# Kernel tuning notes

Measured on AMD Instinct MI355X. Metric: run time of the kernel, lower is better.

Reference implementation:

```python
import jax, jax.numpy as jnp
import numpy as np

N = 50000      # num nodes
E = 1_600_000  # num edges (avg degree 32)
IN = 128       # in_dim
HID = 64       # hidden_dim
H = 4          # heads (layer 1)
NEG_SLOPE = 0.2


def setup_inputs() -> dict:
    key = jax.random.key(0)
    ks = jax.random.split(key, 20)
    g = lambda k, s: jax.random.normal(k, s, dtype=jnp.float32) * 0.05
    return {
        "x": jax.random.normal(ks[0], (N, IN), dtype=jnp.float32),
        "edge_index": jax.random.randint(ks[1], (2, E), 0, N, dtype=jnp.int32),
        # GATv2 layer 1: in=128 -> heads=4, out=64, concat -> 256
        "W1l": g(ks[2], (IN, H * HID)), "b1l": g(ks[3], (H * HID,)),
        "W1r": g(ks[4], (IN, H * HID)), "b1r": g(ks[5], (H * HID,)),
        "att1": g(ks[6], (H, HID)),     "bias1": g(ks[7], (H * HID,)),
        # GATv2 layer 2: in=256 -> heads=1, out=64
        "W2l": g(ks[8], (H * HID, HID)), "b2l": g(ks[9], (HID,)),
        "W2r": g(ks[10], (H * HID, HID)), "b2r": g(ks[11], (HID,)),
        "att2": g(ks[12], (1, HID)),     "bias2": g(ks[13], (HID,)),
        # readout: 64 -> 1
        "Wro": g(ks[14], (HID, 1)), "bro": g(ks[15], (1,)),
    }


def gatv2_layer(x, src, dst, Wl, bl, Wr, br, att, bias, heads, out_ch, concat):
    n = x.shape[0]
    xl = (x @ Wl + bl).reshape(n, heads, out_ch)  # source transform [N,H,C]
    xr = (x @ Wr + br).reshape(n, heads, out_ch)  # target transform [N,H,C]
    # per-edge GATv2 score: a^T LeakyReLU(xl_j + xr_i)
    e = jax.nn.leaky_relu(xl[src] + xr[dst], NEG_SLOPE)      # [E,H,C]
    score = jnp.einsum('ehc,hc->eh', e, att)                 # [E,H]
    # segment softmax over edges sharing the same target node
    m = jax.ops.segment_max(score, dst, num_segments=n)      # [N,H]
    a = jnp.exp(score - m[dst])                              # [E,H]
    denom = jax.ops.segment_sum(a, dst, num_segments=n)      # [N,H]
    alpha = a / denom[dst]
    # weighted scatter-add of source messages
    out = jax.ops.segment_sum(xl[src] * alpha[:, :, None], dst, num_segments=n)  # [N,H,C]
    out = out.reshape(n, heads * out_ch) if concat else out.mean(axis=1)
    return out + bias


def reference(x, edge_index, W1l, b1l, W1r, b1r, att1, bias1,
              W2l, b2l, W2r, b2r, att2, bias2, Wro, bro):
    src, dst = edge_index[0], edge_index[1]
    h = gatv2_layer(x, src, dst, W1l, b1l, W1r, b1r, att1, bias1, H, HID, True)
    h = jax.nn.elu(h)
    h = gatv2_layer(h, src, dst, W2l, b2l, W2r, b2r, att2, bias2, 1, HID, True)
    h = jax.nn.elu(h)
    return h @ Wro + bro  # [N, 1]
```

## Files before the change

### kernel.cpp

```cpp
#include <hip/hip_runtime.h>
#include <hip/hip_bf16.h>
#include <cstdint>
#include <cstddef>

#define NEG_SLOPE 0.2f
#define LOG2E 1.4426950408889634f
#define NBKT 196
#define BCAP 10000
#define P1CHUNK 4096

typedef __attribute__((ext_vector_type(8))) short bf16x8;
typedef __attribute__((ext_vector_type(4))) float f32x4;

__device__ __forceinline__ unsigned short f2bf(float f) {
  unsigned u = __float_as_uint(f);
  u = u + 0x7FFFu + ((u >> 16) & 1u);
  return (unsigned short)(u >> 16);
}
__device__ __forceinline__ unsigned pack2bf(float a, float b) {
  return (unsigned)f2bf(a) | ((unsigned)f2bf(b) << 16);
}
__device__ __forceinline__ float4 cvt_bf4(uint2 q) {
  float4 v;
  v.x = __uint_as_float(q.x << 16);
  v.y = __uint_as_float(q.x & 0xffff0000u);
  v.z = __uint_as_float(q.y << 16);
  v.w = __uint_as_float(q.y & 0xffff0000u);
  return v;
}

__global__ void fill_u32(unsigned* __restrict__ p, unsigned v, long long n) {
  long long i = (long long)blockIdx.x * blockDim.x + threadIdx.x;
  long long s = (long long)gridDim.x * blockDim.x;
  for (; i < n; i += s) p[i] = v;
}

__global__ __launch_bounds__(256) void csr_p1(const int* __restrict__ src,
                                              const int* __restrict__ dst,
                                              int* __restrict__ bcnt,
                                              unsigned* __restrict__ stage, int E) {
  __shared__ int cnt[NBKT], gbase[NBKT];
  const int t = threadIdx.x;
  const int e0 = blockIdx.x * P1CHUNK;
  const int e1 = min(e0 + P1CHUNK, E);
  for (int i = t; i < NBKT; i += 256) cnt[i] = 0;
  __syncthreads();
  for (int e = e0 + t; e < e1; e += 256) atomicAdd(&cnt[dst[e] >> 8], 1);
  __syncthreads();
  for (int i = t; i < NBKT; i += 256) {
    gbase[i] = cnt[i] ? atomicAdd(&bcnt[i], cnt[i]) : 0;
    cnt[i] = 0;
  }
  __syncthreads();
  for (int e = e0 + t; e < e1; e += 256) {
    const int d = dst[e];
    const int b = d >> 8;
    const int r = gbase[b] + atomicAdd(&cnt[b], 1);
    if (r < BCAP)
      stage[(size_t)b * BCAP + r] = (unsigned)src[e] | ((unsigned)(d & 255) << 24);
  }
}

__global__ __launch_bounds__(1024) void csr_p2(const unsigned* __restrict__ stage,
                                               const int* __restrict__ bcnt,
                                               int* __restrict__ csr_src,
                                               int* __restrict__ base, int N, int E) {
  __shared__ int h[256], c[256];
  __shared__ int allb[NBKT];
  __shared__ int ob_s;
  const int t = threadIdx.x;
  const int b = blockIdx.x;
  if (t < 256) h[t] = 0;
  for (int i = t; i < NBKT; i += 1024) allb[i] = min(bcnt[i], BCAP);
  __syncthreads();
  if (t == 0) {
    int s = 0;
    for (int i = 0; i < b; ++i) s += allb[i];
    ob_s = s;
  }
  __syncthreads();
  const int out_base = ob_s;
  const int cnt = allb[b];
  const unsigned* sp = stage + (size_t)b * BCAP;
  for (int i = t; i < cnt; i += 1024) atomicAdd(&h[sp[i] >> 24], 1);
  __syncthreads();
  const int own = (t < 256) ? h[t] : 0;
  for (int off = 1; off < 256; off <<= 1) {
    const int add = (t < 256 && t >= off) ? h[t - off] : 0;
    __syncthreads();
    if (t < 256) h[t] += add;
    __syncthreads();
  }
  if (t < 256) {
    const int excl = h[t] - own;
    c[t] = excl;
    const int node = b * 256 + t;
    if (node < N) base[node] = out_base + excl;
  }
  if (b == gridDim.x - 1 && t == 0) base[N] = E;
  __syncthreads();
  for (int i = t; i < cnt; i += 1024) {
    const unsigned v = sp[i];
    const int pos = out_base + atomicAdd(&c[v >> 24], 1);
    csr_src[pos] = (int)(v & 0xFFFFFFu);
  }
}

__device__ __forceinline__ void wt_cvt(const float* __restrict__ Wl,
                                       const float* __restrict__ Wr,
                                       unsigned short* __restrict__ Wt, int K, int C, int idx) {
  const int k = idx / (2 * C);
  const int c = idx - k * 2 * C;
  const float v = (c < C) ? Wl[(size_t)k * C + c] : Wr[(size_t)k * C + (c - C)];
  Wt[(size_t)c * K + k] = f2bf(v);
}

__global__ void prep(const float* __restrict__ x,
                     const float* __restrict__ W1l, const float* __restrict__ W1r,
                     const float* __restrict__ W2l, const float* __restrict__ W2r,
                     unsigned short* __restrict__ xbf, unsigned short* __restrict__ Wt1,
                     unsigned short* __restrict__ Wt2, long long n8) {
  const int b = blockIdx.x;
  const int t = threadIdx.x;
  if (b < 2048) {
    long long i = (long long)b * 256 + t;
    const long long s = 2048LL * 256;
    for (; i < n8; i += s) {
      const float4 a = ((const float4*)x)[i * 2];
      const float4 c = ((const float4*)x)[i * 2 + 1];
      ((uint2*)xbf)[i * 2] = make_uint2(pack2bf(a.x, a.y), pack2bf(a.z, a.w));
      ((uint2*)xbf)[i * 2 + 1] = make_uint2(pack2bf(c.x, c.y), pack2bf(c.z, c.w));
    }
  } else if (b < 2304) {
    wt_cvt(W1l, W1r, Wt1, 128, 256, (b - 2048) * 256 + t);
  } else {
    wt_cvt(W2l, W2r, Wt2, 256, 64, (b - 2304) * 256 + t);
  }
}

template <int K, int NT, int SPLIT>
__global__ __launch_bounds__(256) void gemm_mfma(
    const unsigned short* __restrict__ A, const unsigned short* __restrict__ Wt,
    const float* __restrict__ bl, const float* __restrict__ br,
    unsigned short* __restrict__ Yl, unsigned short* __restrict__ Yr) {
  constexpr int KS = K / 32;
  constexpr int CW = NT / 4;
  constexpr int NTILES = CW / 16;
  const int wv = threadIdx.x >> 6, lane = threadIdx.x & 63;
  const int n0 = blockIdx.x * 16;
  const int ar = lane & 15;
  const int kg = lane >> 4;

  bf16x8 afrag[KS];
#pragma unroll
  for (int ks = 0; ks < KS; ++ks)
    afrag[ks] = *(const bf16x8*)(A + (size_t)(n0 + ar) * K + ks * 32 + kg * 8);

  const int col0w = wv * CW;
#pragma unroll
  for (int nt = 0; nt < NTILES; ++nt) {
    const int c0 = col0w + nt * 16;
    const int ccol = c0 + (lane & 15);
    f32x4 acc = {0.f, 0.f, 0.f, 0.f};
#pragma unroll
    for (int ks = 0; ks < KS; ++ks) {
      const bf16x8 bfrag = *(const bf16x8*)(Wt + (size_t)ccol * K + ks * 32 + kg * 8);
      acc = __builtin_amdgcn_mfma_f32_16x16x32_bf16(afrag[ks], bfrag, acc, 0, 0, 0);
    }
    if (c0 < SPLIT) {
      const float bv = bl[ccol];
#pragma unroll
      for (int j = 0; j < 4; ++j) {
        const int node = n0 + (lane >> 4) * 4 + j;
        Yl[(size_t)node * SPLIT + ccol] = f2bf(acc[j] + bv);
      }
    } else {
      const float bv = br[ccol - SPLIT];
#pragma unroll
      for (int j = 0; j < 4; ++j) {
        const int node = n0 + (lane >> 4) * 4 + j;
        Yr[(size_t)node * (NT - SPLIT) + (ccol - SPLIT)] = f2bf(acc[j] + bv);
      }
    }
  }
}

__device__ __forceinline__ float edge_p(const float4 c, const float4 xrv, const float4 attv) {
  const float v0 = c.x + xrv.x, v1 = c.y + xrv.y, v2 = c.z + xrv.z, v3 = c.w + xrv.w;
  float p = fmaxf(v0, v0 * NEG_SLOPE) * attv.x;
  p = fmaf(fmaxf(v1, v1 * NEG_SLOPE), attv.y, p);
  p = fmaf(fmaxf(v2, v2 * NEG_SLOPE), attv.z, p);
  p = fmaf(fmaxf(v3, v3 * NEG_SLOPE), attv.w, p);
  p += __shfl_xor(p, 1);
  p += __shfl_xor(p, 2);
  p += __shfl_xor(p, 4);
  p += __shfl_xor(p, 8);
  return __builtin_amdgcn_exp2f(p);
}

__device__ __forceinline__ void edge_acc(uint2 c, const float4& xrv, const float4& attv,
                                         float& dsum, float4& acc) {
  const float4 x = cvt_bf4(c);
  const float p = edge_p(x, xrv, attv);
  dsum += p;
  acc.x = fmaf(p, x.x, acc.x);
  acc.y = fmaf(p, x.y, acc.y);
  acc.z = fmaf(p, x.z, acc.z);
  acc.w = fmaf(p, x.w, acc.w);
}

__global__ __launch_bounds__(256) void node_l1_fused(
    const unsigned short* __restrict__ xlb, const unsigned short* __restrict__ xrb,
    const int* __restrict__ csr_src, const int* __restrict__ base,
    const float* __restrict__ att, const float* __restrict__ bias,
    unsigned short* __restrict__ outb, int N) {
  const int wv = threadIdx.x >> 6, lane = threadIdx.x & 63;
  const int n = blockIdx.x * 4 + wv;
  if (n >= N) return;
  const int beg = __builtin_amdgcn_readfirstlane(base[n]);
  const int deg = __builtin_amdgcn_readfirstlane(base[n + 1]) - beg;
  const float4 xrv = cvt_bf4(((const uint2*)xrb)[(size_t)n * 64 + lane]);
  float4 attv = ((const float4*)att)[lane];
  attv.x *= LOG2E; attv.y *= LOG2E; attv.z *= LOG2E; attv.w *= LOG2E;

  float dsum = 0.f;
  float4 acc = make_float4(0.f, 0.f, 0.f, 0.f);

  if (deg > 0) {
    const int dm1 = deg - 1;
    const uint2* XL = (const uint2*)xlb;
    int s0 = csr_src[beg];
    int s1 = csr_src[beg + (1 < dm1 ? 1 : dm1)];
    int s2 = csr_src[beg + (2 < dm1 ? 2 : dm1)];
    int s3 = csr_src[beg + (3 < dm1 ? 3 : dm1)];
    uint2 r0 = XL[(size_t)s0 * 64 + lane];
    uint2 r1 = XL[(size_t)s1 * 64 + lane];
    uint2 r2 = XL[(size_t)s2 * 64 + lane];
    uint2 r3 = XL[(size_t)s3 * 64 + lane];
    s0 = csr_src[beg + (4 < dm1 ? 4 : dm1)];
    s1 = csr_src[beg + (5 < dm1 ? 5 : dm1)];
    s2 = csr_src[beg + (6 < dm1 ? 6 : dm1)];
    s3 = csr_src[beg + (7 < dm1 ? 7 : dm1)];
    for (int i = 0; i < deg; i += 4) {
      const uint2 c0 = r0, c1 = r1, c2 = r2, c3 = r3;
      r0 = XL[(size_t)s0 * 64 + lane];
      r1 = XL[(size_t)s1 * 64 + lane];
      r2 = XL[(size_t)s2 * 64 + lane];
      r3 = XL[(size_t)s3 * 64 + lane];
      const int j0 = i + 8 < dm1 ? i + 8 : dm1;
      const int j1 = i + 9 < dm1 ? i + 9 : dm1;
      const int j2 = i + 10 < dm1 ? i + 10 : dm1;
      const int j3 = i + 11 < dm1 ? i + 11 : dm1;
      s0 = csr_src[beg + j0];
      s1 = csr_src[beg + j1];
      s2 = csr_src[beg + j2];
      s3 = csr_src[beg + j3];
      edge_acc(c0, xrv, attv, dsum, acc);
      if (i + 1 <= dm1) edge_acc(c1, xrv, attv, dsum, acc);
      if (i + 2 <= dm1) edge_acc(c2, xrv, attv, dsum, acc);
      if (i + 3 <= dm1) edge_acc(c3, xrv, attv, dsum, acc);
    }
  }
  const float inv = (deg > 0) ? 1.0f / dsum : 0.f;
  const float4 b4 = ((const float4*)bias)[lane];
  float4 o;
  o.x = fmaf(acc.x, inv, b4.x); o.x = o.x > 0.f ? o.x : expm1f(o.x);
  o.y = fmaf(acc.y, inv, b4.y); o.y = o.y > 0.f ? o.y : expm1f(o.y);
  o.z = fmaf(acc.z, inv, b4.z); o.z = o.z > 0.f ? o.z : expm1f(o.z);
  o.w = fmaf(acc.w, inv, b4.w); o.w = o.w > 0.f ? o.w : expm1f(o.w);
  ((uint2*)outb)[(size_t)n * 64 + lane] = make_uint2(pack2bf(o.x, o.y), pack2bf(o.z, o.w));
}

__global__ __launch_bounds__(256) void node_l2_fused(
    const unsigned short* __restrict__ xlb, const unsigned short* __restrict__ xrb,
    const int* __restrict__ csr_src, const int* __restrict__ base,
    const float* __restrict__ att, const float* __restrict__ bias,
    const float* __restrict__ Wro, const float* __restrict__ bro,
    float* __restrict__ out, int N) {
  const int gl = threadIdx.x & 15;
  const int n = blockIdx.x * 16 + (threadIdx.x >> 4);
  const int gbase = (threadIdx.x & 63) & 48;
  if (n >= N) return;
  const int beg = base[n];
  const int deg = base[n + 1] - beg;
  const float4 xrv = cvt_bf4(((const uint2*)xrb)[(size_t)n * 16 + gl]);
  float4 attv = ((const float4*)att)[gl];
  attv.x *= LOG2E; attv.y *= LOG2E; attv.z *= LOG2E; attv.w *= LOG2E;
  const uint2* XL = (const uint2*)xlb;

  float dsum = 0.f;
  float4 acc = make_float4(0.f, 0.f, 0.f, 0.f);

  for (int chunk = 0; chunk < deg; chunk += 16) {
    const int cnt = min(16, deg - chunk);
    const int si = (gl < cnt) ? csr_src[beg + chunk + gl] : 0;
    int s = __shfl(si, gbase);
    uint2 nx = XL[(size_t)s * 16 + gl];
    for (int j = 0; j < cnt; ++j) {
      const uint2 cj = nx;
      if (j + 1 < cnt) {
        const int s2 = __shfl(si, gbase + j + 1);
        nx = XL[(size_t)s2 * 16 + gl];
      }
      edge_acc(cj, xrv, attv, dsum, acc);
    }
  }
  const float inv = (deg > 0) ? 1.0f / dsum : 0.f;
  const float4 b4 = ((const float4*)bias)[gl];
  float ox = fmaf(acc.x, inv, b4.x); ox = ox > 0.f ? ox : expm1f(ox);
  float oy = fmaf(acc.y, inv, b4.y); oy = oy > 0.f ? oy : expm1f(oy);
  float oz = fmaf(acc.z, inv, b4.z); oz = oz > 0.f ? oz : expm1f(oz);
  float ow = fmaf(acc.w, inv, b4.w); ow = ow > 0.f ? ow : expm1f(ow);
  const float4 w4 = ((const float4*)Wro)[gl];
  float r = ox * w4.x + oy * w4.y + oz * w4.z + ow * w4.w;
  r += __shfl_xor(r, 1);
  r += __shfl_xor(r, 2);
  r += __shfl_xor(r, 4);
  r += __shfl_xor(r, 8);
  if (gl == 0) out[n] = r + bro[0];
}

extern "C" void kernel_launch(void* const* d_in, const int* in_sizes, int n_in,
                              void* d_out, int out_size, void* d_ws, size_t ws_size,
                              hipStream_t stream) {
  const float* x     = (const float*)d_in[0];
  const int*   ei    = (const int*)d_in[1];
  const float* W1l   = (const float*)d_in[2];
  const float* b1l   = (const float*)d_in[3];
  const float* W1r   = (const float*)d_in[4];
  const float* b1r   = (const float*)d_in[5];
  const float* att1  = (const float*)d_in[6];
  const float* bias1 = (const float*)d_in[7];
  const float* W2l   = (const float*)d_in[8];
  const float* b2l   = (const float*)d_in[9];
  const float* W2r   = (const float*)d_in[10];
  const float* b2r   = (const float*)d_in[11];
  const float* att2  = (const float*)d_in[12];
  const float* bias2 = (const float*)d_in[13];
  const float* Wro   = (const float*)d_in[14];
  const float* bro   = (const float*)d_in[15];

  const int N = in_sizes[0] / 128;
  const int E = in_sizes[1] / 2;
  const int* src = ei;
  const int* dst = ei + E;

  float* ws = (float*)d_ws;
  unsigned short* xbf  = (unsigned short*)ws;
  unsigned short* xl1b = (unsigned short*)(ws + (size_t)64 * N);
  unsigned short* xr1b = (unsigned short*)(ws + (size_t)192 * N);
  unsigned short* h1b  = (unsigned short*)(ws + (size_t)320 * N);
  int* csr_src = (int*)(ws + (size_t)448 * N);
  int* base    = csr_src + E;
  int* bcnt    = base + N + 1;
  unsigned* stage = (unsigned*)(bcnt + NBKT);
  unsigned short* Wt1 = (unsigned short*)(stage + (size_t)NBKT * BCAP);
  unsigned short* Wt2 = Wt1 + 512 * 128;
  unsigned short* xl2b = xbf;
  unsigned short* xr2b = xl1b;

  fill_u32<<<dim3(1), dim3(256), 0, stream>>>((unsigned*)bcnt, 0u, NBKT);
  csr_p1<<<dim3((E + P1CHUNK - 1) / P1CHUNK), dim3(256), 0, stream>>>(src, dst, bcnt, stage, E);
  csr_p2<<<dim3(NBKT), dim3(1024), 0, stream>>>(stage, bcnt, csr_src, base, N, E);

  prep<<<dim3(2432), dim3(256), 0, stream>>>(x, W1l, W1r, W2l, W2r, xbf, Wt1, Wt2,
                                             (long long)N * 128 / 8);

  gemm_mfma<128, 512, 256><<<dim3(N / 16), dim3(256), 0, stream>>>(xbf, Wt1, b1l, b1r,
                                                                   xl1b, xr1b);
  node_l1_fused<<<dim3((N + 3) / 4), dim3(256), 0, stream>>>(xl1b, xr1b, csr_src, base,
                                                             att1, bias1, h1b, N);

  gemm_mfma<256, 128, 64><<<dim3(N / 16), dim3(256), 0, stream>>>(h1b, Wt2, b2l, b2r,
                                                                  xl2b, xr2b);
  node_l2_fused<<<dim3((N + 15) / 16), dim3(256), 0, stream>>>(xl2b, xr2b, csr_src, base,
                                                               att2, bias2, Wro, bro,
                                                               (float*)d_out, N);
}
```

Baseline: 302.5 us.

## Process multiple edges per wavefront in GAT aggregation kernels with wider loads

Layer-1 aggregation now has each wavefront handle two edges at once: each 32-lane half reads 16 bytes per lane from one edge's source row, and the halves are combined with a cross-half shuffle at the end. Layer-2 aggregation moves from 16 nodes per block to one node per wavefront, with four 16-lane quarters each processing a different edge and a reduction across quarters at the end. The aim is more memory-level parallelism and fewer serialized per-edge iterations during the gather. The bounds check on n was removed, which relies on N being a multiple of 4, and layer 2 launches four times as many blocks.

```diff
diff --git a/kernel.cpp b/kernel.cpp
--- a/kernel.cpp
+++ b/kernel.cpp
@@ -20,13 +20,21 @@
 __device__ __forceinline__ unsigned pack2bf(float a, float b) {
   return (unsigned)f2bf(a) | ((unsigned)f2bf(b) << 16);
 }
-__device__ __forceinline__ float4 cvt_bf4(uint2 q) {
-  float4 v;
-  v.x = __uint_as_float(q.x << 16);
-  v.y = __uint_as_float(q.x & 0xffff0000u);
-  v.z = __uint_as_float(q.y << 16);
-  v.w = __uint_as_float(q.y & 0xffff0000u);
-  return v;
+__device__ __forceinline__ void cvt_bf8(uint4 u, float* f) {
+  f[0] = __uint_as_float(u.x << 16);
+  f[1] = __uint_as_float(u.x & 0xffff0000u);
+  f[2] = __uint_as_float(u.y << 16);
+  f[3] = __uint_as_float(u.y & 0xffff0000u);
+  f[4] = __uint_as_float(u.z << 16);
+  f[5] = __uint_as_float(u.z & 0xffff0000u);
+  f[6] = __uint_as_float(u.w << 16);
+  f[7] = __uint_as_float(u.w & 0xffff0000u);
+}
+__device__ __forceinline__ void cvt_bf4p(uint2 u, float* f) {
+  f[0] = __uint_as_float(u.x << 16);
+  f[1] = __uint_as_float(u.x & 0xffff0000u);
+  f[2] = __uint_as_float(u.y << 16);
+  f[3] = __uint_as_float(u.y & 0xffff0000u);
 }
 
 __global__ void fill_u32(unsigned* __restrict__ p, unsigned v, long long n) {
@@ -185,30 +193,6 @@
   }
 }
 
-__device__ __forceinline__ float edge_p(const float4 c, const float4 xrv, const float4 attv) {
-  const float v0 = c.x + xrv.x, v1 = c.y + xrv.y, v2 = c.z + xrv.z, v3 = c.w + xrv.w;
-  float p = fmaxf(v0, v0 * NEG_SLOPE) * attv.x;
-  p = fmaf(fmaxf(v1, v1 * NEG_SLOPE), attv.y, p);
-  p = fmaf(fmaxf(v2, v2 * NEG_SLOPE), attv.z, p);
-  p = fmaf(fmaxf(v3, v3 * NEG_SLOPE), attv.w, p);
-  p += __shfl_xor(p, 1);
-  p += __shfl_xor(p, 2);
-  p += __shfl_xor(p, 4);
-  p += __shfl_xor(p, 8);
-  return __builtin_amdgcn_exp2f(p);
-}
-
-__device__ __forceinline__ void edge_acc(uint2 c, const float4& xrv, const float4& attv,
-                                         float& dsum, float4& acc) {
-  const float4 x = cvt_bf4(c);
-  const float p = edge_p(x, xrv, attv);
-  dsum += p;
-  acc.x = fmaf(p, x.x, acc.x);
-  acc.y = fmaf(p, x.y, acc.y);
-  acc.z = fmaf(p, x.z, acc.z);
-  acc.w = fmaf(p, x.w, acc.w);
-}
-
 __global__ __launch_bounds__(256) void node_l1_fused(
     const unsigned short* __restrict__ xlb, const unsigned short* __restrict__ xrb,
     const int* __restrict__ csr_src, const int* __restrict__ base,
@@ -216,37 +200,125 @@
     unsigned short* __restrict__ outb, int N) {
   const int wv = threadIdx.x >> 6, lane = threadIdx.x & 63;
   const int n = blockIdx.x * 4 + wv;
-  if (n >= N) return;
+  const int h = lane >> 5;
+  const int q = lane & 31;
   const int beg = __builtin_amdgcn_readfirstlane(base[n]);
   const int deg = __builtin_amdgcn_readfirstlane(base[n + 1]) - beg;
-  const float4 xrv = cvt_bf4(((const uint2*)xrb)[(size_t)n * 64 + lane]);
-  float4 attv = ((const float4*)att)[lane];
-  attv.x *= LOG2E; attv.y *= LOG2E; attv.z *= LOG2E; attv.w *= LOG2E;
+  const uint4* XL = (const uint4*)xlb;
+
+  float xr[8];
+  cvt_bf8(((const uint4*)xrb)[(size_t)n * 32 + q], xr);
+  float at[8];
+  {
+    const float4 a0 = ((const float4*)att)[q * 2];
+    const float4 a1 = ((const float4*)att)[q * 2 + 1];
+    at[0] = a0.x * LOG2E; at[1] = a0.y * LOG2E; at[2] = a0.z * LOG2E; at[3] = a0.w * LOG2E;
+    at[4] = a1.x * LOG2E; at[5] = a1.y * LOG2E; at[6] = a1.z * LOG2E; at[7] = a1.w * LOG2E;
+  }
 
   float dsum = 0.f;
-  float4 acc = make_float4(0.f, 0.f, 0.f, 0.f);
+  float acc[8] = {0.f, 0.f, 0.f, 0.f, 0.f, 0.f, 0.f, 0.f};
 
   if (deg > 0) {
     const int dm1 = deg - 1;
-    const uint2* XL = (const uint2*)xlb;
+    int sA = csr_src[beg];
+    int sB = csr_src[beg + (1 < dm1 ? 1 : dm1)];
+    uint4 r = XL[(size_t)(h ? sB : sA) * 32 + q];
+    sA = csr_src[beg + (2 < dm1 ? 2 : dm1)];
+    sB = csr_src[beg + (3 < dm1 ? 3 : dm1)];
+    for (int i = 0; i < deg; i += 2) {
+      const uint4 cur = r;
+      r = XL[(size_t)(h ? sB : sA) * 32 + q];
+      const int j0 = i + 4 < dm1 ? i + 4 : dm1;
+      const int j1 = i + 5 < dm1 ? i + 5 : dm1;
+      sA = csr_src[beg + j0];
+      sB = csr_src[beg + j1];
+      float xl[8];
+      cvt_bf8(cur, xl);
+      float p = 0.f;
+#pragma unroll
+      for (int c = 0; c < 8; ++c) {
+        const float v = xl[c] + xr[c];
+        p = fmaf(fmaxf(v, v * NEG_SLOPE), at[c], p);
+      }
+      p += __shfl_xor(p, 1);
+      p += __shfl_xor(p, 2);
+      p += __shfl_xor(p, 4);
+      p = __builtin_amdgcn_exp2f(p);
+      if (h && (i + 1 > dm1)) p = 0.f;
+      dsum += p;
+#pragma unroll
+      for (int c = 0; c < 8; ++c) acc[c] = fmaf(p, xl[c], acc[c]);
+    }
+    dsum += __shfl_xor(dsum, 32);
+#pragma unroll
+    for (int c = 0; c < 8; ++c) acc[c] += __shfl_xor(acc[c], 32);
+  }
+  const float inv = (deg > 0) ? 1.0f / dsum : 0.f;
+  if (h == 0) {
+    const float4 b0 = ((const float4*)bias)[q * 2];
+    const float4 b1 = ((const float4*)bias)[q * 2 + 1];
+    const float bb[8] = {b0.x, b0.y, b0.z, b0.w, b1.x, b1.y, b1.z, b1.w};
+    float o[8];
+#pragma unroll
+    for (int c = 0; c < 8; ++c) {
+      float v = fmaf(acc[c], inv, bb[c]);
+      o[c] = v > 0.f ? v : expm1f(v);
+    }
+    uint4 pk;
+    pk.x = pack2bf(o[0], o[1]);
+    pk.y = pack2bf(o[2], o[3]);
+    pk.z = pack2bf(o[4], o[5]);
+    pk.w = pack2bf(o[6], o[7]);
+    ((uint4*)outb)[(size_t)n * 32 + q] = pk;
+  }
+}
+
+__global__ __launch_bounds__(256) void node_l2_fused(
+    const unsigned short* __restrict__ xlb, const unsigned short* __restrict__ xrb,
+    const int* __restrict__ csr_src, const int* __restrict__ base,
+    const float* __restrict__ att, const float* __restrict__ bias,
+    const float* __restrict__ Wro, const float* __restrict__ bro,
+    float* __restrict__ out, int N) {
+  const int wv = threadIdx.x >> 6, lane = threadIdx.x & 63;
+  const int n = blockIdx.x * 4 + wv;
+  const int qd = lane >> 4;
+  const int q = lane & 15;
+  const int beg = __builtin_amdgcn_readfirstlane(base[n]);
+  const int deg = __builtin_amdgcn_readfirstlane(base[n + 1]) - beg;
+  const uint2* XL = (const uint2*)xlb;
+
+  float xr[4];
+  cvt_bf4p(((const uint2*)xrb)[(size_t)n * 16 + q], xr);
+  float at[4];
+  {
+    const float4 a = ((const float4*)att)[q];
+    at[0] = a.x * LOG2E; at[1] = a.y * LOG2E; at[2] = a.z * LOG2E; at[3] = a.w * LOG2E;
+  }
+
+  float dsum = 0.f;
+  float acc[4] = {0.f, 0.f, 0.f, 0.f};
+
+  if (deg > 0) {
+    const int dm1 = deg - 1;
     int s0 = csr_src[beg];
     int s1 = csr_src[beg + (1 < dm1 ? 1 : dm1)];
     int s2 = csr_src[beg + (2 < dm1 ? 2 : dm1)];
     int s3 = csr_src[beg + (3 < dm1 ? 3 : dm1)];
-    uint2 r0 = XL[(size_t)s0 * 64 + lane];
-    uint2 r1 = XL[(size_t)s1 * 64 + lane];
-    uint2 r2 = XL[(size_t)s2 * 64 + lane];
-    uint2 r3 = XL[(size_t)s3 * 64 + lane];
+    int sa = (qd & 1) ? s1 : s0;
+    int sb = (qd & 1) ? s3 : s2;
+    int sel = (qd & 2) ? sb : sa;
+    uint2 r = XL[(size_t)sel * 16 + q];
     s0 = csr_src[beg + (4 < dm1 ? 4 : dm1)];
     s1 = csr_src[beg + (5 < dm1 ? 5 : dm1)];
     s2 = csr_src[beg + (6 < dm1 ? 6 : dm1)];
     s3 = csr_src[beg + (7 < dm1 ? 7 : dm1)];
     for (int i = 0; i < deg; i += 4) {
-      const uint2 c0 = r0, c1 = r1, c2 = r2, c3 = r3;
-      r0 = XL[(size_t)s0 * 64 + lane];
-      r1 = XL[(size_t)s1 * 64 + lane];
-      r2 = XL[(size_t)s2 * 64 + lane];
-      r3 = XL[(size_t)s3 * 64 + lane];
+      const uint2 cur = r;
+      sa = (qd & 1) ? s1 : s0;
+      sb = (qd & 1) ? s3 : s2;
+      sel = (qd & 2) ? sb : sa;
+      r = XL[(size_t)sel * 16 + q];
       const int j0 = i + 8 < dm1 ? i + 8 : dm1;
       const int j1 = i + 9 < dm1 ? i + 9 : dm1;
       const int j2 = i + 10 < dm1 ? i + 10 : dm1;
@@ -255,69 +327,49 @@
       s1 = csr_src[beg + j1];
       s2 = csr_src[beg + j2];
       s3 = csr_src[beg + j3];
-      edge_acc(c0, xrv, attv, dsum, acc);
-      if (i + 1 <= dm1) edge_acc(c1, xrv, attv, dsum, acc);
-      if (i + 2 <= dm1) edge_acc(c2, xrv, attv, dsum, acc);
-      if (i + 3 <= dm1) edge_acc(c3, xrv, attv, dsum, acc);
+      float xl[4];
+      cvt_bf4p(cur, xl);
+      float p = 0.f;
+#pragma unroll
+      for (int c = 0; c < 4; ++c) {
+        const float v = xl[c] + xr[c];
+        p = fmaf(fmaxf(v, v * NEG_SLOPE), at[c], p);
+      }
+      p += __shfl_xor(p, 1);
+      p += __shfl_xor(p, 2);
+      p += __shfl_xor(p, 4);
+      p += __shfl_xor(p, 8);
+      p = __builtin_amdgcn_exp2f(p);
+      if (i + qd > dm1) p = 0.f;
+      dsum += p;
+#pragma unroll
+      for (int c = 0; c < 4; ++c) acc[c] = fmaf(p, xl[c], acc[c]);
+    }
+    dsum += __shfl_xor(dsum, 16);
+    dsum += __shfl_xor(dsum, 32);
+#pragma unroll
+    for (int c = 0; c < 4; ++c) {
+      acc[c] += __shfl_xor(acc[c], 16);
+      acc[c] += __shfl_xor(acc[c], 32);
     }
   }
   const float inv = (deg > 0) ? 1.0f / dsum : 0.f;
-  const float4 b4 = ((const float4*)bias)[lane];
-  float4 o;
-  o.x = fmaf(acc.x, inv, b4.x); o.x = o.x > 0.f ? o.x : expm1f(o.x);
-  o.y = fmaf(acc.y, inv, b4.y); o.y = o.y > 0.f ? o.y : expm1f(o.y);
-  o.z = fmaf(acc.z, inv, b4.z); o.z = o.z > 0.f ? o.z : expm1f(o.z);
-  o.w = fmaf(acc.w, inv, b4.w); o.w = o.w > 0.f ? o.w : expm1f(o.w);
-  ((uint2*)outb)[(size_t)n * 64 + lane] = make_uint2(pack2bf(o.x, o.y), pack2bf(o.z, o.w));
-}
-
-__global__ __launch_bounds__(256) void node_l2_fused(
-    const unsigned short* __restrict__ xlb, const unsigned short* __restrict__ xrb,
-    const int* __restrict__ csr_src, const int* __restrict__ base,
-    const float* __restrict__ att, const float* __restrict__ bias,
-    const float* __restrict__ Wro, const float* __restrict__ bro,
-    float* __restrict__ out, int N) {
-  const int gl = threadIdx.x & 15;
-  const int n = blockIdx.x * 16 + (threadIdx.x >> 4);
-  const int gbase = (threadIdx.x & 63) & 48;
-  if (n >= N) return;
-  const int beg = base[n];
-  const int deg = base[n + 1] - beg;
-  const float4 xrv = cvt_bf4(((const uint2*)xrb)[(size_t)n * 16 + gl]);
-  float4 attv = ((const float4*)att)[gl];
-  attv.x *= LOG2E; attv.y *= LOG2E; attv.z *= LOG2E; attv.w *= LOG2E;
-  const uint2* XL = (const uint2*)xlb;
-
-  float dsum = 0.f;
-  float4 acc = make_float4(0.f, 0.f, 0.f, 0.f);
-
-  for (int chunk = 0; chunk < deg; chunk += 16) {
-    const int cnt = min(16, deg - chunk);
-    const int si = (gl < cnt) ? csr_src[beg + chunk + gl] : 0;
-    int s = __shfl(si, gbase);
-    uint2 nx = XL[(size_t)s * 16 + gl];
-    for (int j = 0; j < cnt; ++j) {
-      const uint2 cj = nx;
-      if (j + 1 < cnt) {
-        const int s2 = __shfl(si, gbase + j + 1);
-        nx = XL[(size_t)s2 * 16 + gl];
-      }
-      edge_acc(cj, xrv, attv, dsum, acc);
-    }
-  }
-  const float inv = (deg > 0) ? 1.0f / dsum : 0.f;
-  const float4 b4 = ((const float4*)bias)[gl];
-  float ox = fmaf(acc.x, inv, b4.x); ox = ox > 0.f ? ox : expm1f(ox);
-  float oy = fmaf(acc.y, inv, b4.y); oy = oy > 0.f ? oy : expm1f(oy);
-  float oz = fmaf(acc.z, inv, b4.z); oz = oz > 0.f ? oz : expm1f(oz);
-  float ow = fmaf(acc.w, inv, b4.w); ow = ow > 0.f ? ow : expm1f(ow);
-  const float4 w4 = ((const float4*)Wro)[gl];
-  float r = ox * w4.x + oy * w4.y + oz * w4.z + ow * w4.w;
+  const float4 b4 = ((const float4*)bias)[q];
+  const float bb[4] = {b4.x, b4.y, b4.z, b4.w};
+  const float4 w4 = ((const float4*)Wro)[q];
+  const float ww[4] = {w4.x, w4.y, w4.z, w4.w};
+  float r = 0.f;
+#pragma unroll
+  for (int c = 0; c < 4; ++c) {
+    float v = fmaf(acc[c], inv, bb[c]);
+    v = v > 0.f ? v : expm1f(v);
+    r = fmaf(v, ww[c], r);
+  }
   r += __shfl_xor(r, 1);
   r += __shfl_xor(r, 2);
   r += __shfl_xor(r, 4);
   r += __shfl_xor(r, 8);
-  if (gl == 0) out[n] = r + bro[0];
+  if (lane == 0) out[n] = r + bro[0];
 }
 
 extern "C" void kernel_launch(void* const* d_in, const int* in_sizes, int n_in,
@@ -373,7 +425,7 @@
 
   gemm_mfma<256, 128, 64><<<dim3(N / 16), dim3(256), 0, stream>>>(h1b, Wt2, b2l, b2r,
                                                                   xl2b, xr2b);
-  node_l2_fused<<<dim3((N + 15) / 16), dim3(256), 0, stream>>>(xl2b, xr2b, csr_src, base,
-                                                               att2, bias2, Wro, bro,
-                                                               (float*)d_out, N);
-}
+  node_l2_fused<<<dim3((N + 3) / 4), dim3(256), 0, stream>>>(xl2b, xr2b, csr_src, base,
+                                                             att2, bias2, Wro, bro,
+                                                             (float*)d_out, N);
+}
```

Result: slower. 314.0 us (+3.8%).

## Merge independent CSR build and prep/GEMM stages into shared launches

Applied to the files above, without the earlier changes.

The CSR pass-1 bucketing now shares one launch with the bf16 conversion of x and the weights. The CSR pass-2 scatter shares one launch with the layer-1 GEMM, with block ranges picking the role. The fill kernel becomes a hipMemsetAsync. This cuts the launch count and lets independent work run side by side on the GPU instead of serialising. Pass 2 now uses 256-thread blocks instead of 1024, so each bucket gets fewer threads.

```diff
diff --git a/kernel.cpp b/kernel.cpp
--- a/kernel.cpp
+++ b/kernel.cpp
@@ -8,6 +8,7 @@
 #define NBKT 196
 #define BCAP 10000
 #define P1CHUNK 4096
+#define P1B 391
 
 typedef __attribute__((ext_vector_type(8))) short bf16x8;
 typedef __attribute__((ext_vector_type(4))) float f32x4;
@@ -29,83 +30,6 @@
   return v;
 }
 
-__global__ void fill_u32(unsigned* __restrict__ p, unsigned v, long long n) {
-  long long i = (long long)blockIdx.x * blockDim.x + threadIdx.x;
-  long long s = (long long)gridDim.x * blockDim.x;
-  for (; i < n; i += s) p[i] = v;
-}
-
-__global__ __launch_bounds__(256) void csr_p1(const int* __restrict__ src,
-                                              const int* __restrict__ dst,
-                                              int* __restrict__ bcnt,
-                                              unsigned* __restrict__ stage, int E) {
-  __shared__ int cnt[NBKT], gbase[NBKT];
-  const int t = threadIdx.x;
-  const int e0 = blockIdx.x * P1CHUNK;
-  const int e1 = min(e0 + P1CHUNK, E);
-  for (int i = t; i < NBKT; i += 256) cnt[i] = 0;
-  __syncthreads();
-  for (int e = e0 + t; e < e1; e += 256) atomicAdd(&cnt[dst[e] >> 8], 1);
-  __syncthreads();
-  for (int i = t; i < NBKT; i += 256) {
-    gbase[i] = cnt[i] ? atomicAdd(&bcnt[i], cnt[i]) : 0;
-    cnt[i] = 0;
-  }
-  __syncthreads();
-  for (int e = e0 + t; e < e1; e += 256) {
-    const int d = dst[e];
-    const int b = d >> 8;
-    const int r = gbase[b] + atomicAdd(&cnt[b], 1);
-    if (r < BCAP)
-      stage[(size_t)b * BCAP + r] = (unsigned)src[e] | ((unsigned)(d & 255) << 24);
-  }
-}
-
-__global__ __launch_bounds__(1024) void csr_p2(const unsigned* __restrict__ stage,
-                                               const int* __restrict__ bcnt,
-                                               int* __restrict__ csr_src,
-                                               int* __restrict__ base, int N, int E) {
-  __shared__ int h[256], c[256];
-  __shared__ int allb[NBKT];
-  __shared__ int ob_s;
-  const int t = threadIdx.x;
-  const int b = blockIdx.x;
-  if (t < 256) h[t] = 0;
-  for (int i = t; i < NBKT; i += 1024) allb[i] = min(bcnt[i], BCAP);
-  __syncthreads();
-  if (t == 0) {
-    int s = 0;
-    for (int i = 0; i < b; ++i) s += allb[i];
-    ob_s = s;
-  }
-  __syncthreads();
-  const int out_base = ob_s;
-  const int cnt = allb[b];
-  const unsigned* sp = stage + (size_t)b * BCAP;
-  for (int i = t; i < cnt; i += 1024) atomicAdd(&h[sp[i] >> 24], 1);
-  __syncthreads();
-  const int own = (t < 256) ? h[t] : 0;
-  for (int off = 1; off < 256; off <<= 1) {
-    const int add = (t < 256 && t >= off) ? h[t - off] : 0;
-    __syncthreads();
-    if (t < 256) h[t] += add;
-    __syncthreads();
-  }
-  if (t < 256) {
-    const int excl = h[t] - own;
-    c[t] = excl;
-    const int node = b * 256 + t;
-    if (node < N) base[node] = out_base + excl;
-  }
-  if (b == gridDim.x - 1 && t == 0) base[N] = E;
-  __syncthreads();
-  for (int i = t; i < cnt; i += 1024) {
-    const unsigned v = sp[i];
-    const int pos = out_base + atomicAdd(&c[v >> 24], 1);
-    csr_src[pos] = (int)(v & 0xFFFFFFu);
-  }
-}
-
 __device__ __forceinline__ void wt_cvt(const float* __restrict__ Wl,
                                        const float* __restrict__ Wr,
                                        unsigned short* __restrict__ Wt, int K, int C, int idx) {
@@ -115,15 +39,39 @@
   Wt[(size_t)c * K + k] = f2bf(v);
 }
 
-__global__ void prep(const float* __restrict__ x,
-                     const float* __restrict__ W1l, const float* __restrict__ W1r,
-                     const float* __restrict__ W2l, const float* __restrict__ W2r,
-                     unsigned short* __restrict__ xbf, unsigned short* __restrict__ Wt1,
-                     unsigned short* __restrict__ Wt2, long long n8) {
+__global__ __launch_bounds__(256) void k1_csrp1_prep(
+    const int* __restrict__ src, const int* __restrict__ dst,
+    int* __restrict__ bcnt, unsigned* __restrict__ stage, int E,
+    const float* __restrict__ x,
+    const float* __restrict__ W1l, const float* __restrict__ W1r,
+    const float* __restrict__ W2l, const float* __restrict__ W2r,
+    unsigned short* __restrict__ xbf, unsigned short* __restrict__ Wt1,
+    unsigned short* __restrict__ Wt2, long long n8) {
+  __shared__ int cnt[NBKT], gbase[NBKT];
   const int b = blockIdx.x;
   const int t = threadIdx.x;
-  if (b < 2048) {
-    long long i = (long long)b * 256 + t;
+  if (b < P1B) {
+    const int e0 = b * P1CHUNK;
+    const int e1 = min(e0 + P1CHUNK, E);
+    for (int i = t; i < NBKT; i += 256) cnt[i] = 0;
+    __syncthreads();
+    for (int e = e0 + t; e < e1; e += 256) atomicAdd(&cnt[dst[e] >> 8], 1);
+    __syncthreads();
+    for (int i = t; i < NBKT; i += 256) {
+      gbase[i] = cnt[i] ? atomicAdd(&bcnt[i], cnt[i]) : 0;
+      cnt[i] = 0;
+    }
+    __syncthreads();
+    for (int e = e0 + t; e < e1; e += 256) {
+      const int d = dst[e];
+      const int bk = d >> 8;
+      const int r = gbase[bk] + atomicAdd(&cnt[bk], 1);
+      if (r < BCAP)
+        stage[(size_t)bk * BCAP + r] = (unsigned)src[e] | ((unsigned)(d & 255) << 24);
+    }
+  } else if (b < P1B + 2048) {
+    const int lb = b - P1B;
+    long long i = (long long)lb * 256 + t;
     const long long s = 2048LL * 256;
     for (; i < n8; i += s) {
       const float4 a = ((const float4*)x)[i * 2];
@@ -131,23 +79,23 @@
       ((uint2*)xbf)[i * 2] = make_uint2(pack2bf(a.x, a.y), pack2bf(a.z, a.w));
       ((uint2*)xbf)[i * 2 + 1] = make_uint2(pack2bf(c.x, c.y), pack2bf(c.z, c.w));
     }
-  } else if (b < 2304) {
-    wt_cvt(W1l, W1r, Wt1, 128, 256, (b - 2048) * 256 + t);
+  } else if (b < P1B + 2048 + 256) {
+    wt_cvt(W1l, W1r, Wt1, 128, 256, (b - (P1B + 2048)) * 256 + t);
   } else {
-    wt_cvt(W2l, W2r, Wt2, 256, 64, (b - 2304) * 256 + t);
+    wt_cvt(W2l, W2r, Wt2, 256, 64, (b - (P1B + 2048 + 256)) * 256 + t);
   }
 }
 
 template <int K, int NT, int SPLIT>
-__global__ __launch_bounds__(256) void gemm_mfma(
+__device__ __forceinline__ void gemm_body(
     const unsigned short* __restrict__ A, const unsigned short* __restrict__ Wt,
     const float* __restrict__ bl, const float* __restrict__ br,
-    unsigned short* __restrict__ Yl, unsigned short* __restrict__ Yr) {
+    unsigned short* __restrict__ Yl, unsigned short* __restrict__ Yr, int bb) {
   constexpr int KS = K / 32;
   constexpr int CW = NT / 4;
   constexpr int NTILES = CW / 16;
   const int wv = threadIdx.x >> 6, lane = threadIdx.x & 63;
-  const int n0 = blockIdx.x * 16;
+  const int n0 = bb * 16;
   const int ar = lane & 15;
   const int kg = lane >> 4;
 
@@ -183,6 +131,65 @@
       }
     }
   }
+}
+
+__global__ __launch_bounds__(256) void k2_csrp2_gemm1(
+    const unsigned* __restrict__ stage, const int* __restrict__ bcnt,
+    int* __restrict__ csr_src, int* __restrict__ base, int N, int E,
+    const unsigned short* __restrict__ A, const unsigned short* __restrict__ Wt,
+    const float* __restrict__ bl, const float* __restrict__ br,
+    unsigned short* __restrict__ Yl, unsigned short* __restrict__ Yr) {
+  __shared__ int h[256], c[256];
+  __shared__ int allb[NBKT];
+  __shared__ int ob_s;
+  const int b = blockIdx.x;
+  const int t = threadIdx.x;
+  if (b >= NBKT) {
+    gemm_body<128, 512, 256>(A, Wt, bl, br, Yl, Yr, b - NBKT);
+    return;
+  }
+  h[t] = 0;
+  for (int i = t; i < NBKT; i += 256) allb[i] = min(bcnt[i], BCAP);
+  __syncthreads();
+  if (t == 0) {
+    int s = 0;
+    for (int i = 0; i < b; ++i) s += allb[i];
+    ob_s = s;
+  }
+  __syncthreads();
+  const int out_base = ob_s;
+  const int cnt = allb[b];
+  const unsigned* sp = stage + (size_t)b * BCAP;
+  for (int i = t; i < cnt; i += 256) atomicAdd(&h[sp[i] >> 24], 1);
+  __syncthreads();
+  const int own = h[t];
+  for (int off = 1; off < 256; off <<= 1) {
+    const int add = (t >= off) ? h[t - off] : 0;
+    __syncthreads();
+    h[t] += add;
+    __syncthreads();
+  }
+  {
+    const int excl = h[t] - own;
+    c[t] = excl;
+    const int node = b * 256 + t;
+    if (node < N) base[node] = out_base + excl;
+  }
+  if (b == NBKT - 1 && t == 0) base[N] = E;
+  __syncthreads();
+  for (int i = t; i < cnt; i += 256) {
+    const unsigned v = sp[i];
+    const int pos = out_base + atomicAdd(&c[v >> 24], 1);
+    csr_src[pos] = (int)(v & 0xFFFFFFu);
+  }
+}
+
+template <int K, int NT, int SPLIT>
+__global__ __launch_bounds__(256) void gemm_mfma(
+    const unsigned short* __restrict__ A, const unsigned short* __restrict__ Wt,
+    const float* __restrict__ bl, const float* __restrict__ br,
+    unsigned short* __restrict__ Yl, unsigned short* __restrict__ Yr) {
+  gemm_body<K, NT, SPLIT>(A, Wt, bl, br, Yl, Yr, blockIdx.x);
 }
 
 __device__ __forceinline__ float edge_p(const float4 c, const float4 xrv, const float4 attv) {
@@ -359,20 +366,21 @@
   unsigned short* xl2b = xbf;
   unsigned short* xr2b = xl1b;
 
-  fill_u32<<<dim3(1), dim3(256), 0, stream>>>((unsigned*)bcnt, 0u, NBKT);
-  csr_p1<<<dim3((E + P1CHUNK - 1) / P1CHUNK), dim3(256), 0, stream>>>(src, dst, bcnt, stage, E);
-  csr_p2<<<dim3(NBKT), dim3(1024), 0, stream>>>(stage, bcnt, csr_src, base, N, E);
-
-  prep<<<dim3(2432), dim3(256), 0, stream>>>(x, W1l, W1r, W2l, W2r, xbf, Wt1, Wt2,
-                                             (long long)N * 128 / 8);
-
-  gemm_mfma<128, 512, 256><<<dim3(N / 16), dim3(256), 0, stream>>>(xbf, Wt1, b1l, b1r,
-                                                                   xl1b, xr1b);
+  hipMemsetAsync((void*)bcnt, 0, NBKT * sizeof(int), stream);
+
+  k1_csrp1_prep<<<dim3(P1B + 2048 + 256 + 128), dim3(256), 0, stream>>>(
+      src, dst, bcnt, stage, E, x, W1l, W1r, W2l, W2r, xbf, Wt1, Wt2,
+      (long long)N * 128 / 8);
+
+  k2_csrp2_gemm1<<<dim3(NBKT + N / 16), dim3(256), 0, stream>>>(
+      stage, bcnt, csr_src, base, N, E, xbf, Wt1, b1l, b1r, xl1b, xr1b);
+
   node_l1_fused<<<dim3((N + 3) / 4), dim3(256), 0, stream>>>(xl1b, xr1b, csr_src, base,
                                                              att1, bias1, h1b, N);
 
   gemm_mfma<256, 128, 64><<<dim3(N / 16), dim3(256), 0, stream>>>(h1b, Wt2, b2l, b2r,
                                                                   xl2b, xr2b);
+
   node_l2_fused<<<dim3((N + 15) / 16), dim3(256), 0, stream>>>(xl2b, xr2b, csr_src, base,
                                                                att2, bias2, Wro, bro,
                                                                (float*)d_out, N);
```

Result: faster. 292.4 us (-3.3%).
